# Optimization experiments

Hardware: AMD Instinct MI355X
Metric: run time of the kernel (lower is better)

Reference implementation:

```python
import jax, jax.numpy as jnp
import numpy as np

B, N, F, K, H = 2, 1024, 64, 8, 4
M1 = K + 1                # 9
M2 = (F - 1) * K + 1      # 505
TEMP = 1.0


def setup_inputs() -> dict:
    key = jax.random.key(0)
    ks = jax.random.split(key, 8)
    x = jax.random.normal(ks[0], (B, N, F), dtype=jnp.float32)
    # Bernoulli(0.05) dense adjacency
    adj = (jax.random.uniform(ks[1], (B, N, N)) < 0.05).astype(jnp.float32)
    mask = jnp.ones((B, N), dtype=jnp.float32)
    Wl = jax.random.normal(ks[2], (F, K * H), dtype=jnp.float32) * 0.05
    bl = jnp.zeros((K * H,), dtype=jnp.float32)
    Wr = jax.random.normal(ks[3], (F, K * H), dtype=jnp.float32) * 0.05
    br = jnp.zeros((K * H,), dtype=jnp.float32)
    # fixed affine layer: y = x @ aff_w + aff_b, aff_w[:, :F] = -I, aff_b[M2] = 1
    aff_w = jnp.zeros((F, M1 * M2), dtype=jnp.float32).at[:, :F].set(-jnp.eye(F, dtype=jnp.float32))
    aff_b = jnp.zeros((M1 * M2,), dtype=jnp.float32).at[M2].set(1.0)
    Wm = jax.random.normal(ks[4], (M1 * M2, F), dtype=jnp.float32) * 0.02
    bm = jnp.zeros((F,), dtype=jnp.float32)
    return dict(x=x, adj=adj, mask=mask, Wl=Wl, bl=bl, Wr=Wr, br=br,
                aff_w=aff_w, aff_b=aff_b, Wm=Wm, bm=bm)


def reference(x, adj, mask, Wl, bl, Wr, br, aff_w, aff_b, Wm, bm):
    # --- multi-head edge attention ---
    x_l = (x @ Wl + bl).reshape(B, N, K, H)   # [B,N,K,H]
    x_r = (x @ Wr + br).reshape(B, N, K, H)
    # scores[b,i,j,n,g] = leaky_relu(x_l[b,j] + x_r[b,i]) / temp
    scores = jax.nn.leaky_relu(x_l[:, None, :, :, :] + x_r[:, :, None, :, :]) / TEMP  # [B,N,N,K,H]
    attn_mask = mask[:, None, :] * mask[:, :, None]                # [B,N,N]
    scores = jnp.where(attn_mask[..., None, None] == 0, -1e9, scores)
    att = jax.nn.softmax(scores, axis=2)                           # softmax over source nodes j
    att = jnp.maximum(att * adj[..., None, None], 1e-6)            # clamp(min=1e-6) STE trick
    att = att / jnp.sum(att, axis=2, keepdims=True)                # renormalize
    # --- attention-weighted neighbor gather ---
    x_h = x.reshape(B, N, H, F // H)
    agg = jnp.einsum('bjgk,bijng->bingk', x_h, att).reshape(B, N, K, F)  # [B,N,K,F]
    # --- fixed affine + FFT log-domain geometric mean ---
    x_aff = (agg @ aff_w + aff_b).reshape(B, N, K, M1, M2)
    x_fft = jnp.fft.fft2(x_aff)                                    # over (M1,M2)
    mag = jnp.exp(jnp.mean(jnp.log(jnp.abs(x_fft) + 1e-6), axis=2))  # [B,N,M1,M2]
    ang = jnp.sum(jnp.angle(x_fft), axis=2)
    x_agg = jnp.fft.ifft2(mag * jnp.exp(1j * ang)).real.reshape(B, N, M1 * M2)
    # --- output MLP + node mask ---
    out = x_agg @ Wm + bm
    return out * mask[..., None]
```

## Files before the change

### kernel.cpp

```cpp
#include <hip/hip_runtime.h>
#include <math.h>

#define NN 1024
#define FD 64
#define CH 32
#define M1D 9
#define M2D 505
#define QH 253
#define THALF 2273
#define KPAD 4608
#define KSPLIT 16
#define KCHUNK 288
#define G1SZ 291456
#define G1KS 8

#define FSQRT(x) __builtin_amdgcn_sqrtf(x)
#define FRCP(x)  __builtin_amdgcn_rcpf(x)

typedef short short8 __attribute__((ext_vector_type(8)));
typedef float f32x4 __attribute__((ext_vector_type(4)));

__device__ __forceinline__ unsigned short f2bf(float x) {
    unsigned int u = __builtin_bit_cast(unsigned int, x);
    return (unsigned short)((u + 0x7FFFu + ((u >> 16) & 1u)) >> 16);
}

#define OFF_WP    1024
#define OFF_SUMX  1056
#define OFF_GMT   1184
#define OFF_XL    148640
#define OFF_XR    214176
#define OFF_AGG   279712
#define OFF_PART  1328288
#define OFF_Y     3425440
#define OFF_WT    8144032
#define OFF_G1P   8176800

__global__ __launch_bounds__(256) void build_tw_kernel(float* __restrict__ T,
                                                       float* __restrict__ Wt,
                                                       float* __restrict__ wp,
                                                       float* __restrict__ sumx) {
    int idx = blockIdx.x * 256 + threadIdx.x;
    if (blockIdx.x == 0) {
        if (threadIdx.x < M1D) {
            float ang = (float)threadIdx.x * (-6.2831853f / 9.0f);
            float s, c; __sincosf(ang, &s, &c);
            wp[2*threadIdx.x] = c; wp[2*threadIdx.x+1] = s;
        }
        if (threadIdx.x >= 64 && threadIdx.x < 192) sumx[threadIdx.x - 64] = 0.f;
    }
    if (idx < 506 * 512) {
        int r = idx >> 9, m2 = idx & 511;
        float v = 0.f;
        if (m2 < M2D) {
            int q = r >> 1;
            int t = (q * m2) % M2D;
            float ang = (float)t * (-6.2831853f / 505.0f);
            float s, c; __sincosf(ang, &s, &c);
            v = (r & 1) ? -s : c;
        }
        T[idx] = v;
    } else if (idx < 506 * 512 + 64 * 512) {
        int i2 = idx - 506 * 512;
        int m = i2 >> 9, col = i2 & 511;
        float v = 0.f;
        if (col < 506) {
            int q = col >> 1;
            int t = (q * m) % M2D;
            float ang = (float)t * (-6.2831853f / 505.0f);
            float s, c; __sincosf(ang, &s, &c);
            v = (col & 1) ? s : c;
        }
        Wt[i2] = v;
    }
}

__global__ __launch_bounds__(64) void proj_kernel(const float* __restrict__ x,
                                                  const float* __restrict__ Wl, const float* __restrict__ bl,
                                                  const float* __restrict__ Wr, const float* __restrict__ br,
                                                  float* __restrict__ xl, float* __restrict__ xr,
                                                  float* __restrict__ sumx) {
    int blk = blockIdx.x, tid = threadIdx.x;
    if (blk >= 2048) {
        int bb = blk - 2048;
        int b = bb >> 4, chunk = bb & 15;
        const float* xb = x + (size_t)b * NN * FD;
        float acc = 0.f;
        int j0 = chunk * 64;
        #pragma unroll 4
        for (int j = j0; j < j0 + 64; j++) acc += xb[j*FD + tid];
        atomicAdd(&sumx[b*FD + tid], acc);
        return;
    }
    int node = blk;
    __shared__ float xrow[FD];
    xrow[tid] = x[(size_t)node*FD + tid];
    __syncthreads();
    int c = tid & 31;
    const float* W = (tid < 32) ? Wl : Wr;
    float acc = (tid < 32) ? bl[c] : br[c];
    #pragma unroll
    for (int f = 0; f < FD; f++) acc += xrow[f] * W[f*CH + c];
    float* dst = (tid < 32) ? xl : xr;
    dst[(size_t)node*CH + c] = acc;
}

__global__ __launch_bounds__(256) void g1_gemm_kernel(const float* __restrict__ T,
                                                      const float* __restrict__ Wm,
                                                      float* __restrict__ G1p) {
    int mt = blockIdx.x, m1 = blockIdx.y, ks = blockIdx.z;
    int tid = threadIdx.x;
    __shared__ float As[64][68];
    __shared__ float Bs[64][64];
    int r0 = mt * 64, k0 = ks * 64;
    const float* Wmb = Wm + (size_t)m1 * M2D * FD;
    float ra[16], rb[16];
    #pragma unroll
    for (int i = 0; i < 16; i++) {
        int l = tid + i*256;
        int r = l >> 6, k = l & 63;
        int rr = r0 + r;
        ra[i] = (rr < 506) ? T[(size_t)rr*512 + k0 + k] : 0.f;
    }
    #pragma unroll
    for (int i = 0; i < 16; i++) {
        int l = tid + i*256;
        int k = l >> 6, f = l & 63;
        int krow = k0 + k;
        rb[i] = (krow < M2D) ? Wmb[(size_t)krow*FD + f] : 0.f;
    }
    #pragma unroll
    for (int i = 0; i < 16; i++) {
        int l = tid + i*256;
        As[l & 63][l >> 6] = ra[i];
    }
    #pragma unroll
    for (int i = 0; i < 16; i++) {
        int l = tid + i*256;
        Bs[l >> 6][l & 63] = rb[i];
    }
    __syncthreads();
    float acc[4][4] = {{0.f}};
    int tm = (tid >> 4) * 4, tf = (tid & 15) * 4;
    #pragma unroll 8
    for (int k = 0; k < 64; k++) {
        float4 a = *(const float4*)&As[k][tm];
        float4 b = *(const float4*)&Bs[k][tf];
        acc[0][0] += a.x*b.x; acc[0][1] += a.x*b.y; acc[0][2] += a.x*b.z; acc[0][3] += a.x*b.w;
        acc[1][0] += a.y*b.x; acc[1][1] += a.y*b.y; acc[1][2] += a.y*b.z; acc[1][3] += a.y*b.w;
        acc[2][0] += a.z*b.x; acc[2][1] += a.z*b.y; acc[2][2] += a.z*b.z; acc[2][3] += a.z*b.w;
        acc[3][0] += a.w*b.x; acc[3][1] += a.w*b.y; acc[3][2] += a.w*b.z; acc[3][3] += a.w*b.w;
    }
    float* G1k = G1p + (size_t)ks * G1SZ;
    #pragma unroll
    for (int i = 0; i < 4; i++) {
        int r = r0 + tm + i;
        if (r >= 506) continue;
        int q = r >> 1, reim = r & 1;
        size_t base = (size_t)(m1*QH + q) * 128;
        #pragma unroll
        for (int j = 0; j < 4; j++)
            G1k[base + (tf + j)*2 + reim] = acc[i][j];
    }
}

__global__ __launch_bounds__(64) void gmat_kernel(const float* __restrict__ G1p,
                                                  const float* __restrict__ wp,
                                                  unsigned short* __restrict__ GmT) {
    int t = blockIdx.x;
    int f = threadIdx.x;
    if (t >= THALF) {
        *(unsigned int*)&GmT[(size_t)f*KPAD + 2*t] = 0u;
        return;
    }
    int p, q;
    if (t < QH) { p = 0; q = t; }
    else { int u = t - QH; p = 1 + u / M2D; q = u % M2D; }
    int qq = (q < QH) ? q : (M2D - q);
    float sgn = (q < QH) ? 1.f : -1.f;
    float gr = 0.f, gi = 0.f;
    #pragma unroll
    for (int m1 = 0; m1 < M1D; m1++) {
        size_t o = ((size_t)(m1*QH + qq)*FD + f)*2;
        float ar = 0.f, ai = 0.f;
        #pragma unroll
        for (int ks = 0; ks < G1KS; ks++) {
            ar += G1p[(size_t)ks*G1SZ + o];
            ai += G1p[(size_t)ks*G1SZ + o + 1];
        }
        ai *= sgn;
        int pm = (p * m1) % M1D;
        float cr = wp[2*pm], ci = -wp[2*pm+1];
        gr += ar*cr - ai*ci;
        gi += ar*ci + ai*cr;
    }
    float scale = (t == 0) ? (1.0f/4545.0f) : (2.0f/4545.0f);
    unsigned int pk = (unsigned int)f2bf(gr*scale) | ((unsigned int)f2bf(-gi*scale) << 16);
    *(unsigned int*)&GmT[(size_t)f*KPAD + 2*t] = pk;
}

__global__ __launch_bounds__(256) void attn_agg_kernel(const float* __restrict__ x,
                                                       const float* __restrict__ adj,
                                                       const float* __restrict__ xl,
                                                       const float* __restrict__ xr,
                                                       const float* __restrict__ sumx,
                                                       float* __restrict__ agg) {
    int node = blockIdx.x;
    int b = node >> 10;
    int tid = threadIdx.x;
    __shared__ float xr_s[CH], Zinv[CH], Sinv[CH];
    __shared__ float red16[16][CH];
    __shared__ int act_list[NN + 8];
    __shared__ int act_n;
    __shared__ float qv2[64][CH];

    if (tid < CH) xr_s[tid] = xr[(size_t)node*CH + tid];
    if (tid == 0) act_n = 0;
    __syncthreads();

    int c = tid & 31, jl = tid >> 5;
    const float* xlb = xl + ((size_t)b << 10) * CH;
    const float* adjrow = adj + (size_t)node * NN;

    int c2 = tid & 15, jl16 = tid >> 4;
    const float2* xlb2 = (const float2*)xlb;
    float xrcx = xr_s[2*c2], xrcy = xr_s[2*c2+1];
    float zx = 0.f, zy = 0.f;
    for (int j0 = jl16; j0 < NN; j0 += 128) {
        float2 sv[8];
        #pragma unroll
        for (int u = 0; u < 8; u++) sv[u] = xlb2[(size_t)(j0 + u*16)*16 + c2];
        #pragma unroll
        for (int u = 0; u < 8; u++) {
            float s0 = sv[u].x + xrcx; s0 = s0 > 0.f ? s0 : 0.01f * s0;
            float s1 = sv[u].y + xrcy; s1 = s1 > 0.f ? s1 : 0.01f * s1;
            zx += __expf(s0); zy += __expf(s1);
        }
    }
    red16[jl16][2*c2]   = zx;
    red16[jl16][2*c2+1] = zy;

    float av[4];
    #pragma unroll
    for (int u = 0; u < 4; u++) av[u] = adjrow[tid + u*256];
    __syncthreads();
    if (tid < CH) {
        float z = 0.f;
        #pragma unroll
        for (int r = 0; r < 16; r++) z += red16[r][tid];
        Zinv[tid] = FRCP(z);
    }
    #pragma unroll
    for (int u = 0; u < 4; u++)
        if (av[u] != 0.f) { int p = atomicAdd(&act_n, 1); act_list[p] = tid + u*256; }
    __syncthreads();
    int nact = act_n;

    int f = tid & 63, n0 = tid >> 6;
    int g = f >> 4;
    int c0 = n0*4 + g, c1 = (n0+4)*4 + g;
    const float* xb = x + ((size_t)b << 10) * FD;
    float acc0 = 0.f, acc1 = 0.f, sacc = 0.f;

    for (int base = 0; base < nact; base += 64) {
        int cnt = min(64, nact - base);
        int cntp = (cnt + 7) & ~7;
        for (int u = tid; u < (cnt << 5); u += 256) {
            int jj = u >> 5, cc = u & 31;
            int j = act_list[base + jj];
            float s = xlb[j*CH + cc] + xr_s[cc];
            s = s > 0.f ? s : 0.01f * s;
            float pv = __expf(s) * Zinv[cc];
            float qq = fmaxf(pv, 1e-6f) - 1e-6f;
            qv2[jj][cc] = qq;
            sacc += qq;
        }
        for (int u = tid + (cnt << 5); u < (cntp << 5); u += 256)
            qv2[u >> 5][u & 31] = 0.f;
        if (tid < cntp - cnt) act_list[base + cnt + tid] = act_list[base];
        __syncthreads();
        for (int jb = 0; jb < cntp; jb += 8) {
            float xv[8];
            #pragma unroll
            for (int u = 0; u < 8; u++) xv[u] = xb[act_list[base + jb + u]*FD + f];
            #pragma unroll
            for (int u = 0; u < 8; u++) {
                acc0 += qv2[jb+u][c0] * xv[u];
                acc1 += qv2[jb+u][c1] * xv[u];
            }
        }
        __syncthreads();
    }
    red16[jl][c] = sacc;
    __syncthreads();
    if (tid < CH) {
        float s = 0.f;
        #pragma unroll
        for (int r = 0; r < 8; r++) s += red16[r][tid];
        Sinv[tid] = FRCP(s + (float)NN * 1e-6f);
    }
    __syncthreads();
    float sx = sumx[b*FD + f] * 1e-6f;
    agg[(size_t)node*512 + n0*FD + f]       = (acc0 + sx) * Sinv[c0];
    agg[(size_t)node*512 + (n0+4)*FD + f]   = (acc1 + sx) * Sinv[c1];
}

__global__ __launch_bounds__(256) void ay_kernel(const float* __restrict__ agg,
                                                 const float* __restrict__ Wt,
                                                 unsigned short* __restrict__ Yb) {
    int slab = blockIdx.x, nt = blockIdx.y;
    int tid = threadIdx.x;
    __shared__ float As2[64][68];
    __shared__ float Bs[64][64];
    int tm = (tid >> 4) * 4, tf = (tid & 15) * 4;
    float ra[16], rb[16];
    #pragma unroll
    for (int i = 0; i < 16; i++) {
        int l = tid + i*256;
        int r = l >> 6, k = l & 63;
        ra[i] = agg[(size_t)(slab*64 + r)*64 + k];
    }
    #pragma unroll
    for (int i = 0; i < 16; i++) {
        int l = tid + i*256;
        int k = l >> 6, cc = l & 63;
        rb[i] = Wt[(size_t)k*512 + nt*64 + cc];
    }
    #pragma unroll
    for (int i = 0; i < 16; i++) { int l = tid + i*256; As2[l & 63][l >> 6] = ra[i]; }
    #pragma unroll
    for (int i = 0; i < 16; i++) { int l = tid + i*256; Bs[l >> 6][l & 63] = rb[i]; }
    __syncthreads();
    float acc[4][4] = {{0.f}};
    #pragma unroll 8
    for (int k = 0; k < 64; k++) {
        float4 a = *(const float4*)&As2[k][tm];
        float4 b = *(const float4*)&Bs[k][tf];
        acc[0][0] += a.x*b.x; acc[0][1] += a.x*b.y; acc[0][2] += a.x*b.z; acc[0][3] += a.x*b.w;
        acc[1][0] += a.y*b.x; acc[1][1] += a.y*b.y; acc[1][2] += a.y*b.z; acc[1][3] += a.y*b.w;
        acc[2][0] += a.z*b.x; acc[2][1] += a.z*b.y; acc[2][2] += a.z*b.z; acc[2][3] += a.z*b.w;
        acc[3][0] += a.w*b.x; acc[3][1] += a.w*b.y; acc[3][2] += a.w*b.z; acc[3][3] += a.w*b.w;
    }
    __syncthreads();
    #pragma unroll
    for (int i = 0; i < 4; i++)
        #pragma unroll
        for (int j = 0; j < 4; j++)
            As2[tm + i][tf + j] = acc[i][j];
    __syncthreads();

    int qloc = tid & 31, node = tid >> 5;
    unsigned short* Yrow = Yb + (size_t)(slab*8 + node)*KPAD;
    int q = nt*32 + qloc;

    if (q <= 252) {
        float2 Av[8];
        #pragma unroll
        for (int n = 0; n < 8; n++)
            Av[n] = make_float2(As2[node*8 + n][2*qloc], As2[node*8 + n][2*qloc + 1]);

        const float CPt[5] = {1.0f, 0.766044443119f, 0.173648177667f, -0.5f, -0.939692620786f};
        const float SPt[5] = {0.0f, -0.642787609687f, -0.984807753012f, -0.866025403784f, -0.342020143326f};

        #define Y_PROD(CSIGN, TIDX)                                            \
        {                                                                      \
            float Pr = 1.f, Pi = 0.f, rp2 = 1.f;                               \
            _Pragma("unroll")                                                  \
            for (int n = 0; n < 8; n++) {                                      \
                float Xr = cp - Av[n].x, Xi = sp - (CSIGN) * Av[n].y;          \
                rp2 *= (Xr*Xr + Xi*Xi);                                        \
                float nPr = Pr*Xr - Pi*Xi;                                     \
                Pi = Pr*Xi + Pi*Xr; Pr = nPr;                                  \
            }                                                                  \
            float pAbs = FSQRT(Pr*Pr + Pi*Pi);                                 \
            float rp8 = FSQRT(FSQRT(FSQRT(FSQRT(rp2))));                       \
            float s = rp8 * FRCP(fmaxf(pAbs, 1e-20f));                         \
            unsigned int pk = (unsigned int)f2bf(s*Pr) | ((unsigned int)f2bf(s*Pi) << 16); \
            *(unsigned int*)&Yrow[2*(TIDX)] = pk;                              \
        }

        #pragma unroll
        for (int p = 0; p < 5; p++) {
            float cp = CPt[p], sp = SPt[p];
            int tfwd = (p == 0) ? q : (QH + (p-1)*M2D + q);
            Y_PROD(1.f, tfwd);
            if (p >= 1 && q >= 1) {
                int tmir = QH + (p-1)*M2D + (M2D - q);
                Y_PROD(-1.f, tmir);
            }
        }
        #undef Y_PROD
    }
    if (nt == 7 && tid < 248) {
        int rr = tid / 31, cc2 = tid % 31;
        unsigned short* Yr2 = Yb + (size_t)(slab*8 + rr)*KPAD;
        *(unsigned int*)&Yr2[2*THALF + 2*cc2] = 0u;
    }
}

__global__ __launch_bounds__(256) void gemm_kernel(const unsigned short* __restrict__ Yb,
                                                   const unsigned short* __restrict__ GmT,
                                                   float* __restrict__ part) {
    int mtile = blockIdx.x, kc = blockIdx.y;
    int tid = threadIdx.x;
    __shared__ unsigned short Ys[64*40];
    __shared__ unsigned short Gs[64*40];
    int m0 = mtile * 64;
    int k0 = kc * KCHUNK;
    int r = tid >> 2, kg = (tid & 3) * 8;
    const unsigned short* Ysrc = Yb + (size_t)(m0 + r)*KPAD + k0 + kg;
    const unsigned short* Gsrc = GmT + (size_t)r*KPAD + k0 + kg;
    uint4 ya = *(const uint4*)Ysrc;
    uint4 ga = *(const uint4*)Gsrc;
    int w = tid >> 6, lane = tid & 63;
    int lm = lane & 15, quad = lane >> 4;
    f32x4 acc0 = {0.f,0.f,0.f,0.f}, acc1 = acc0, acc2 = acc0, acc3 = acc0;
    for (int ks = 0; ks < KCHUNK; ks += 32) {
        *(uint4*)&Ys[r*40 + kg] = ya;
        *(uint4*)&Gs[r*40 + kg] = ga;
        __syncthreads();
        if (ks + 32 < KCHUNK) {
            ya = *(const uint4*)(Ysrc + ks + 32);
            ga = *(const uint4*)(Gsrc + ks + 32);
        }
        short8 b  = *(const short8*)&Gs[(w*16 + lm)*40 + quad*8];
        short8 a0 = *(const short8*)&Ys[(lm)*40      + quad*8];
        short8 a1 = *(const short8*)&Ys[(16 + lm)*40 + quad*8];
        short8 a2 = *(const short8*)&Ys[(32 + lm)*40 + quad*8];
        short8 a3 = *(const short8*)&Ys[(48 + lm)*40 + quad*8];
        acc0 = __builtin_amdgcn_mfma_f32_16x16x32_bf16(a0, b, acc0, 0, 0, 0);
        acc1 = __builtin_amdgcn_mfma_f32_16x16x32_bf16(a1, b, acc1, 0, 0, 0);
        acc2 = __builtin_amdgcn_mfma_f32_16x16x32_bf16(a2, b, acc2, 0, 0, 0);
        acc3 = __builtin_amdgcn_mfma_f32_16x16x32_bf16(a3, b, acc3, 0, 0, 0);
        __syncthreads();
    }
    float* prow = part + (size_t)kc * (2048*FD);
    int col = w*16 + lm;
    #pragma unroll
    for (int rr = 0; rr < 4; rr++) {
        int row = quad*4 + rr;
        prow[(size_t)(m0 + row)*FD + col]      = acc0[rr];
        prow[(size_t)(m0 + 16 + row)*FD + col] = acc1[rr];
        prow[(size_t)(m0 + 32 + row)*FD + col] = acc2[rr];
        prow[(size_t)(m0 + 48 + row)*FD + col] = acc3[rr];
    }
}

__global__ __launch_bounds__(256) void reduce_kernel(const float* __restrict__ part,
                                                     const float* __restrict__ bm,
                                                     const float* __restrict__ mask,
                                                     float* __restrict__ out) {
    int idx = blockIdx.x * 256 + threadIdx.x;
    if (idx >= 32768) return;
    const float4* p4 = (const float4*)part;
    float4 s = p4[idx];
    #pragma unroll
    for (int kc = 1; kc < KSPLIT; kc++) {
        float4 v = p4[(size_t)kc*32768 + idx];
        s.x += v.x; s.y += v.y; s.z += v.z; s.w += v.w;
    }
    int f0 = (idx & 15) * 4;
    int node = idx >> 4;
    float mk = mask[node];
    s.x = (s.x + bm[f0])   * mk;
    s.y = (s.y + bm[f0+1]) * mk;
    s.z = (s.z + bm[f0+2]) * mk;
    s.w = (s.w + bm[f0+3]) * mk;
    ((float4*)out)[idx] = s;
}

extern "C" void kernel_launch(void* const* d_in, const int* in_sizes, int n_in,
                              void* d_out, int out_size, void* d_ws, size_t ws_size,
                              hipStream_t stream) {
    const float* x    = (const float*)d_in[0];
    const float* adj  = (const float*)d_in[1];
    const float* mask = (const float*)d_in[2];
    const float* Wl   = (const float*)d_in[3];
    const float* bl   = (const float*)d_in[4];
    const float* Wr   = (const float*)d_in[5];
    const float* br   = (const float*)d_in[6];
    const float* Wm   = (const float*)d_in[9];
    const float* bm   = (const float*)d_in[10];
    float* out = (float*)d_out;
    float* ws  = (float*)d_ws;

    float* wp   = ws + OFF_WP;
    float* sumx = ws + OFF_SUMX;
    unsigned short* GmT = (unsigned short*)(ws + OFF_GMT);
    float* xl   = ws + OFF_XL;
    float* xr   = ws + OFF_XR;
    float* agg  = ws + OFF_AGG;
    float* part = ws + OFF_PART;
    float* T    = ws + OFF_Y;
    unsigned short* Yb = (unsigned short*)(ws + OFF_Y);
    float* Wt   = ws + OFF_WT;
    float* G1p  = ws + OFF_G1P;

    hipLaunchKernelGGL(build_tw_kernel, dim3((506*512 + 64*512 + 255)/256), dim3(256), 0, stream, T, Wt, wp, sumx);
    hipLaunchKernelGGL(proj_kernel, dim3(2080), dim3(64), 0, stream, x, Wl, bl, Wr, br, xl, xr, sumx);
    hipLaunchKernelGGL(g1_gemm_kernel, dim3(8, 9, G1KS), dim3(256), 0, stream, T, Wm, G1p);
    hipLaunchKernelGGL(gmat_kernel, dim3(KPAD/2), dim3(64), 0, stream, G1p, wp, GmT);
    hipLaunchKernelGGL(attn_agg_kernel, dim3(2048), dim3(256), 0, stream, x, adj, xl, xr, sumx, agg);
    hipLaunchKernelGGL(ay_kernel, dim3(256, 8), dim3(256), 0, stream, agg, Wt, Yb);
    hipLaunchKernelGGL(gemm_kernel, dim3(32, KSPLIT), dim3(256), 0, stream, Yb, GmT, part);
    hipLaunchKernelGGL(reduce_kernel, dim3(128), dim3(256), 0, stream, part, bm, mask, out);
}
```

Before: 177.7 us.

## Fuse pipeline into four launches with inline twiddles and atomic split-K output

Eight kernel launches become four. The twiddle-table build moves inline, so twiddles are computed with sincos inside the G1 GEMM and ay tiles. The projection, column-sum, G1 GEMM and output-bias initialisation share one grid, and gmat shares a grid with the attention kernel. The separate split-K reduce kernel is removed: gemm_kernel atomically adds masked partials into an output pre-filled with bias. The intent is to cut launch overhead and intermediate global traffic. The cost is extra transcendental work, float atomic contention, and non-deterministic summation order.

```diff
diff --git a/kernel.cpp b/kernel.cpp
--- a/kernel.cpp
+++ b/kernel.cpp
@@ -25,189 +25,170 @@
     return (unsigned short)((u + 0x7FFFu + ((u >> 16) & 1u)) >> 16);
 }
 
-#define OFF_WP    1024
-#define OFF_SUMX  1056
-#define OFF_GMT   1184
-#define OFF_XL    148640
-#define OFF_XR    214176
-#define OFF_AGG   279712
-#define OFF_PART  1328288
-#define OFF_Y     3425440
-#define OFF_WT    8144032
-#define OFF_G1P   8176800
-
-__global__ __launch_bounds__(256) void build_tw_kernel(float* __restrict__ T,
-                                                       float* __restrict__ Wt,
-                                                       float* __restrict__ wp,
-                                                       float* __restrict__ sumx) {
-    int idx = blockIdx.x * 256 + threadIdx.x;
-    if (blockIdx.x == 0) {
-        if (threadIdx.x < M1D) {
-            float ang = (float)threadIdx.x * (-6.2831853f / 9.0f);
-            float s, c; __sincosf(ang, &s, &c);
-            wp[2*threadIdx.x] = c; wp[2*threadIdx.x+1] = s;
-        }
-        if (threadIdx.x >= 64 && threadIdx.x < 192) sumx[threadIdx.x - 64] = 0.f;
-    }
-    if (idx < 506 * 512) {
-        int r = idx >> 9, m2 = idx & 511;
-        float v = 0.f;
-        if (m2 < M2D) {
-            int q = r >> 1;
-            int t = (q * m2) % M2D;
-            float ang = (float)t * (-6.2831853f / 505.0f);
-            float s, c; __sincosf(ang, &s, &c);
-            v = (r & 1) ? -s : c;
-        }
-        T[idx] = v;
-    } else if (idx < 506 * 512 + 64 * 512) {
-        int i2 = idx - 506 * 512;
-        int m = i2 >> 9, col = i2 & 511;
-        float v = 0.f;
-        if (col < 506) {
-            int q = col >> 1;
-            int t = (q * m) % M2D;
-            float ang = (float)t * (-6.2831853f / 505.0f);
-            float s, c; __sincosf(ang, &s, &c);
-            v = (col & 1) ? s : c;
-        }
-        Wt[i2] = v;
-    }
-}
-
-__global__ __launch_bounds__(64) void proj_kernel(const float* __restrict__ x,
-                                                  const float* __restrict__ Wl, const float* __restrict__ bl,
-                                                  const float* __restrict__ Wr, const float* __restrict__ br,
-                                                  float* __restrict__ xl, float* __restrict__ xr,
-                                                  float* __restrict__ sumx) {
-    int blk = blockIdx.x, tid = threadIdx.x;
-    if (blk >= 2048) {
-        int bb = blk - 2048;
+#define OFF_SUMXP 1024
+#define OFF_GMT   4096
+#define OFF_XL    151552
+#define OFF_XR    217088
+#define OFF_AGG   282624
+#define OFF_Y     1331200
+#define OFF_G1P   6049792
+
+__global__ __launch_bounds__(256) void fused_pre_kernel(
+    const float* __restrict__ x,
+    const float* __restrict__ Wl, const float* __restrict__ bl,
+    const float* __restrict__ Wr, const float* __restrict__ br,
+    const float* __restrict__ Wm, const float* __restrict__ bm,
+    const float* __restrict__ mask,
+    float* __restrict__ xl, float* __restrict__ xr,
+    float* __restrict__ sumxp, float* __restrict__ G1p,
+    float* __restrict__ out)
+{
+    __shared__ float As[64][68];
+    __shared__ float Bs[64][64];
+    int bid = blockIdx.x, tid = threadIdx.x;
+
+    if (bid < 576) {
+        int mt = bid & 7, m1 = (bid >> 3) % 9, ks = bid / 72;
+        int r0 = mt * 64, k0 = ks * 64;
+        const float* Wmb = Wm + (size_t)m1 * M2D * FD;
+        float ra[16], rb[16];
+        #pragma unroll
+        for (int i = 0; i < 16; i++) {
+            int l = tid + i*256;
+            int r = l >> 6, k = l & 63;
+            int rr = r0 + r, m2 = k0 + k;
+            float v = 0.f;
+            if (rr < 506 && m2 < M2D) {
+                int q = rr >> 1;
+                int t = (q * m2) % M2D;
+                float ang = (float)t * (-6.2831853f / 505.0f);
+                float s, c; __sincosf(ang, &s, &c);
+                v = (rr & 1) ? -s : c;
+            }
+            ra[i] = v;
+        }
+        #pragma unroll
+        for (int i = 0; i < 16; i++) {
+            int l = tid + i*256;
+            int k = l >> 6, f = l & 63;
+            int krow = k0 + k;
+            rb[i] = (krow < M2D) ? Wmb[(size_t)krow*FD + f] : 0.f;
+        }
+        #pragma unroll
+        for (int i = 0; i < 16; i++) {
+            int l = tid + i*256;
+            As[l & 63][l >> 6] = ra[i];
+        }
+        #pragma unroll
+        for (int i = 0; i < 16; i++) {
+            int l = tid + i*256;
+            Bs[l >> 6][l & 63] = rb[i];
+        }
+        __syncthreads();
+        float acc[4][4] = {{0.f}};
+        int tm = (tid >> 4) * 4, tf = (tid & 15) * 4;
+        #pragma unroll 8
+        for (int k = 0; k < 64; k++) {
+            float4 a = *(const float4*)&As[k][tm];
+            float4 b = *(const float4*)&Bs[k][tf];
+            acc[0][0] += a.x*b.x; acc[0][1] += a.x*b.y; acc[0][2] += a.x*b.z; acc[0][3] += a.x*b.w;
+            acc[1][0] += a.y*b.x; acc[1][1] += a.y*b.y; acc[1][2] += a.y*b.z; acc[1][3] += a.y*b.w;
+            acc[2][0] += a.z*b.x; acc[2][1] += a.z*b.y; acc[2][2] += a.z*b.z; acc[2][3] += a.z*b.w;
+            acc[3][0] += a.w*b.x; acc[3][1] += a.w*b.y; acc[3][2] += a.w*b.z; acc[3][3] += a.w*b.w;
+        }
+        float* G1k = G1p + (size_t)ks * G1SZ;
+        #pragma unroll
+        for (int i = 0; i < 4; i++) {
+            int r = r0 + tm + i;
+            if (r >= 506) continue;
+            int q = r >> 1, reim = r & 1;
+            size_t base = (size_t)(m1*QH + q) * 128;
+            #pragma unroll
+            for (int j = 0; j < 4; j++)
+                G1k[base + (tf + j)*2 + reim] = acc[i][j];
+        }
+    } else if (bid < 1088) {
+        int grp = tid >> 6, lt = tid & 63;
+        int node = (bid - 576)*4 + grp;
+        float* xrow = &As[0][0] + grp*FD;
+        xrow[lt] = x[(size_t)node*FD + lt];
+        __syncthreads();
+        int c = lt & 31;
+        const float* W = (lt < 32) ? Wl : Wr;
+        float acc = (lt < 32) ? bl[c] : br[c];
+        #pragma unroll
+        for (int f = 0; f < FD; f++) acc += xrow[f] * W[f*CH + c];
+        float* dst = (lt < 32) ? xl : xr;
+        dst[(size_t)node*CH + c] = acc;
+    } else if (bid < 1096) {
+        int bb = (bid - 1088)*4 + (tid >> 6);
+        int f = tid & 63;
         int b = bb >> 4, chunk = bb & 15;
         const float* xb = x + (size_t)b * NN * FD;
         float acc = 0.f;
         int j0 = chunk * 64;
         #pragma unroll 4
-        for (int j = j0; j < j0 + 64; j++) acc += xb[j*FD + tid];
-        atomicAdd(&sumx[b*FD + tid], acc);
+        for (int j = j0; j < j0 + 64; j++) acc += xb[j*FD + f];
+        sumxp[bb*64 + f] = acc;
+    } else {
+        int idx = (bid - 1096)*256 + tid;
+        float4 bv = ((const float4*)bm)[idx & 15];
+        float mk = mask[idx >> 4];
+        bv.x *= mk; bv.y *= mk; bv.z *= mk; bv.w *= mk;
+        ((float4*)out)[idx] = bv;
+    }
+}
+
+__global__ __launch_bounds__(256) void fused_mid_kernel(
+    const float* __restrict__ x, const float* __restrict__ adj,
+    const float* __restrict__ xl, const float* __restrict__ xr,
+    const float* __restrict__ sumxp, const float* __restrict__ G1p,
+    float* __restrict__ agg, unsigned short* __restrict__ GmT)
+{
+    int bid = blockIdx.x, tid = threadIdx.x;
+
+    if (bid >= 2048) {
+        __shared__ float wps[18];
+        if (tid < 9) {
+            float s, c; __sincosf((float)tid * (-6.2831853f / 9.0f), &s, &c);
+            wps[2*tid] = c; wps[2*tid+1] = s;
+        }
+        __syncthreads();
+        int t = (bid - 2048)*4 + (tid >> 6);
+        int f = tid & 63;
+        if (t >= THALF) {
+            *(unsigned int*)&GmT[(size_t)f*KPAD + 2*t] = 0u;
+            return;
+        }
+        int p, q;
+        if (t < QH) { p = 0; q = t; }
+        else { int u = t - QH; p = 1 + u / M2D; q = u % M2D; }
+        int qq = (q < QH) ? q : (M2D - q);
+        float sgn = (q < QH) ? 1.f : -1.f;
+        float gr = 0.f, gi = 0.f;
+        #pragma unroll
+        for (int m1 = 0; m1 < M1D; m1++) {
+            size_t o = ((size_t)(m1*QH + qq)*FD + f)*2;
+            float ar = 0.f, ai = 0.f;
+            #pragma unroll
+            for (int ks = 0; ks < G1KS; ks++) {
+                ar += G1p[(size_t)ks*G1SZ + o];
+                ai += G1p[(size_t)ks*G1SZ + o + 1];
+            }
+            ai *= sgn;
+            int pm = (p * m1) % M1D;
+            float cr = wps[2*pm], ci = -wps[2*pm+1];
+            gr += ar*cr - ai*ci;
+            gi += ar*ci + ai*cr;
+        }
+        float scale = (t == 0) ? (1.0f/4545.0f) : (2.0f/4545.0f);
+        unsigned int pk = (unsigned int)f2bf(gr*scale) | ((unsigned int)f2bf(-gi*scale) << 16);
+        *(unsigned int*)&GmT[(size_t)f*KPAD + 2*t] = pk;
         return;
     }
-    int node = blk;
-    __shared__ float xrow[FD];
-    xrow[tid] = x[(size_t)node*FD + tid];
-    __syncthreads();
-    int c = tid & 31;
-    const float* W = (tid < 32) ? Wl : Wr;
-    float acc = (tid < 32) ? bl[c] : br[c];
-    #pragma unroll
-    for (int f = 0; f < FD; f++) acc += xrow[f] * W[f*CH + c];
-    float* dst = (tid < 32) ? xl : xr;
-    dst[(size_t)node*CH + c] = acc;
-}
-
-__global__ __launch_bounds__(256) void g1_gemm_kernel(const float* __restrict__ T,
-                                                      const float* __restrict__ Wm,
-                                                      float* __restrict__ G1p) {
-    int mt = blockIdx.x, m1 = blockIdx.y, ks = blockIdx.z;
-    int tid = threadIdx.x;
-    __shared__ float As[64][68];
-    __shared__ float Bs[64][64];
-    int r0 = mt * 64, k0 = ks * 64;
-    const float* Wmb = Wm + (size_t)m1 * M2D * FD;
-    float ra[16], rb[16];
-    #pragma unroll
-    for (int i = 0; i < 16; i++) {
-        int l = tid + i*256;
-        int r = l >> 6, k = l & 63;
-        int rr = r0 + r;
-        ra[i] = (rr < 506) ? T[(size_t)rr*512 + k0 + k] : 0.f;
-    }
-    #pragma unroll
-    for (int i = 0; i < 16; i++) {
-        int l = tid + i*256;
-        int k = l >> 6, f = l & 63;
-        int krow = k0 + k;
-        rb[i] = (krow < M2D) ? Wmb[(size_t)krow*FD + f] : 0.f;
-    }
-    #pragma unroll
-    for (int i = 0; i < 16; i++) {
-        int l = tid + i*256;
-        As[l & 63][l >> 6] = ra[i];
-    }
-    #pragma unroll
-    for (int i = 0; i < 16; i++) {
-        int l = tid + i*256;
-        Bs[l >> 6][l & 63] = rb[i];
-    }
-    __syncthreads();
-    float acc[4][4] = {{0.f}};
-    int tm = (tid >> 4) * 4, tf = (tid & 15) * 4;
-    #pragma unroll 8
-    for (int k = 0; k < 64; k++) {
-        float4 a = *(const float4*)&As[k][tm];
-        float4 b = *(const float4*)&Bs[k][tf];
-        acc[0][0] += a.x*b.x; acc[0][1] += a.x*b.y; acc[0][2] += a.x*b.z; acc[0][3] += a.x*b.w;
-        acc[1][0] += a.y*b.x; acc[1][1] += a.y*b.y; acc[1][2] += a.y*b.z; acc[1][3] += a.y*b.w;
-        acc[2][0] += a.z*b.x; acc[2][1] += a.z*b.y; acc[2][2] += a.z*b.z; acc[2][3] += a.z*b.w;
-        acc[3][0] += a.w*b.x; acc[3][1] += a.w*b.y; acc[3][2] += a.w*b.z; acc[3][3] += a.w*b.w;
-    }
-    float* G1k = G1p + (size_t)ks * G1SZ;
-    #pragma unroll
-    for (int i = 0; i < 4; i++) {
-        int r = r0 + tm + i;
-        if (r >= 506) continue;
-        int q = r >> 1, reim = r & 1;
-        size_t base = (size_t)(m1*QH + q) * 128;
-        #pragma unroll
-        for (int j = 0; j < 4; j++)
-            G1k[base + (tf + j)*2 + reim] = acc[i][j];
-    }
-}
-
-__global__ __launch_bounds__(64) void gmat_kernel(const float* __restrict__ G1p,
-                                                  const float* __restrict__ wp,
-                                                  unsigned short* __restrict__ GmT) {
-    int t = blockIdx.x;
-    int f = threadIdx.x;
-    if (t >= THALF) {
-        *(unsigned int*)&GmT[(size_t)f*KPAD + 2*t] = 0u;
-        return;
-    }
-    int p, q;
-    if (t < QH) { p = 0; q = t; }
-    else { int u = t - QH; p = 1 + u / M2D; q = u % M2D; }
-    int qq = (q < QH) ? q : (M2D - q);
-    float sgn = (q < QH) ? 1.f : -1.f;
-    float gr = 0.f, gi = 0.f;
-    #pragma unroll
-    for (int m1 = 0; m1 < M1D; m1++) {
-        size_t o = ((size_t)(m1*QH + qq)*FD + f)*2;
-        float ar = 0.f, ai = 0.f;
-        #pragma unroll
-        for (int ks = 0; ks < G1KS; ks++) {
-            ar += G1p[(size_t)ks*G1SZ + o];
-            ai += G1p[(size_t)ks*G1SZ + o + 1];
-        }
-        ai *= sgn;
-        int pm = (p * m1) % M1D;
-        float cr = wp[2*pm], ci = -wp[2*pm+1];
-        gr += ar*cr - ai*ci;
-        gi += ar*ci + ai*cr;
-    }
-    float scale = (t == 0) ? (1.0f/4545.0f) : (2.0f/4545.0f);
-    unsigned int pk = (unsigned int)f2bf(gr*scale) | ((unsigned int)f2bf(-gi*scale) << 16);
-    *(unsigned int*)&GmT[(size_t)f*KPAD + 2*t] = pk;
-}
-
-__global__ __launch_bounds__(256) void attn_agg_kernel(const float* __restrict__ x,
-                                                       const float* __restrict__ adj,
-                                                       const float* __restrict__ xl,
-                                                       const float* __restrict__ xr,
-                                                       const float* __restrict__ sumx,
-                                                       float* __restrict__ agg) {
-    int node = blockIdx.x;
+
+    int node = bid;
     int b = node >> 10;
-    int tid = threadIdx.x;
     __shared__ float xr_s[CH], Zinv[CH], Sinv[CH];
     __shared__ float red16[16][CH];
     __shared__ int act_list[NN + 8];
@@ -300,13 +281,15 @@
         Sinv[tid] = FRCP(s + (float)NN * 1e-6f);
     }
     __syncthreads();
-    float sx = sumx[b*FD + f] * 1e-6f;
+    float sx = 0.f;
+    #pragma unroll
+    for (int cchunk = 0; cchunk < 16; cchunk++) sx += sumxp[(b*16 + cchunk)*64 + f];
+    sx *= 1e-6f;
     agg[(size_t)node*512 + n0*FD + f]       = (acc0 + sx) * Sinv[c0];
     agg[(size_t)node*512 + (n0+4)*FD + f]   = (acc1 + sx) * Sinv[c1];
 }
 
 __global__ __launch_bounds__(256) void ay_kernel(const float* __restrict__ agg,
-                                                 const float* __restrict__ Wt,
                                                  unsigned short* __restrict__ Yb) {
     int slab = blockIdx.x, nt = blockIdx.y;
     int tid = threadIdx.x;
@@ -324,7 +307,16 @@
     for (int i = 0; i < 16; i++) {
         int l = tid + i*256;
         int k = l >> 6, cc = l & 63;
-        rb[i] = Wt[(size_t)k*512 + nt*64 + cc];
+        int col = nt*64 + cc;
+        float v = 0.f;
+        if (col < 506) {
+            int q = col >> 1;
+            int tt = (q * k) % M2D;
+            float ang = (float)tt * (-6.2831853f / 505.0f);
+            float s, c; __sincosf(ang, &s, &c);
+            v = (col & 1) ? s : c;
+        }
+        rb[i] = v;
     }
     #pragma unroll
     for (int i = 0; i < 16; i++) { int l = tid + i*256; As2[l & 63][l >> 6] = ra[i]; }
@@ -400,7 +392,8 @@
 
 __global__ __launch_bounds__(256) void gemm_kernel(const unsigned short* __restrict__ Yb,
                                                    const unsigned short* __restrict__ GmT,
-                                                   float* __restrict__ part) {
+                                                   const float* __restrict__ mask,
+                                                   float* __restrict__ out) {
     int mtile = blockIdx.x, kc = blockIdx.y;
     int tid = threadIdx.x;
     __shared__ unsigned short Ys[64*40];
@@ -434,39 +427,15 @@
         acc3 = __builtin_amdgcn_mfma_f32_16x16x32_bf16(a3, b, acc3, 0, 0, 0);
         __syncthreads();
     }
-    float* prow = part + (size_t)kc * (2048*FD);
     int col = w*16 + lm;
     #pragma unroll
     for (int rr = 0; rr < 4; rr++) {
-        int row = quad*4 + rr;
-        prow[(size_t)(m0 + row)*FD + col]      = acc0[rr];
-        prow[(size_t)(m0 + 16 + row)*FD + col] = acc1[rr];
-        prow[(size_t)(m0 + 32 + row)*FD + col] = acc2[rr];
-        prow[(size_t)(m0 + 48 + row)*FD + col] = acc3[rr];
-    }
-}
-
-__global__ __launch_bounds__(256) void reduce_kernel(const float* __restrict__ part,
-                                                     const float* __restrict__ bm,
-                                                     const float* __restrict__ mask,
-                                                     float* __restrict__ out) {
-    int idx = blockIdx.x * 256 + threadIdx.x;
-    if (idx >= 32768) return;
-    const float4* p4 = (const float4*)part;
-    float4 s = p4[idx];
-    #pragma unroll
-    for (int kc = 1; kc < KSPLIT; kc++) {
-        float4 v = p4[(size_t)kc*32768 + idx];
-        s.x += v.x; s.y += v.y; s.z += v.z; s.w += v.w;
-    }
-    int f0 = (idx & 15) * 4;
-    int node = idx >> 4;
-    float mk = mask[node];
-    s.x = (s.x + bm[f0])   * mk;
-    s.y = (s.y + bm[f0+1]) * mk;
-    s.z = (s.z + bm[f0+2]) * mk;
-    s.w = (s.w + bm[f0+3]) * mk;
-    ((float4*)out)[idx] = s;
+        int row = m0 + quad*4 + rr;
+        atomicAdd(&out[(size_t)row*FD + col],        acc0[rr] * mask[row]);
+        atomicAdd(&out[(size_t)(row+16)*FD + col],   acc1[rr] * mask[row+16]);
+        atomicAdd(&out[(size_t)(row+32)*FD + col],   acc2[rr] * mask[row+32]);
+        atomicAdd(&out[(size_t)(row+48)*FD + col],   acc3[rr] * mask[row+48]);
+    }
 }
 
 extern "C" void kernel_launch(void* const* d_in, const int* in_sizes, int n_in,
@@ -484,24 +453,18 @@
     float* out = (float*)d_out;
     float* ws  = (float*)d_ws;
 
-    float* wp   = ws + OFF_WP;
-    float* sumx = ws + OFF_SUMX;
+    float* sumxp = ws + OFF_SUMXP;
     unsigned short* GmT = (unsigned short*)(ws + OFF_GMT);
     float* xl   = ws + OFF_XL;
     float* xr   = ws + OFF_XR;
     float* agg  = ws + OFF_AGG;
-    float* part = ws + OFF_PART;
-    float* T    = ws + OFF_Y;
     unsigned short* Yb = (unsigned short*)(ws + OFF_Y);
-    float* Wt   = ws + OFF_WT;
     float* G1p  = ws + OFF_G1P;
 
-    hipLaunchKernelGGL(build_tw_kernel, dim3((506*512 + 64*512 + 255)/256), dim3(256), 0, stream, T, Wt, wp, sumx);
-    hipLaunchKernelGGL(proj_kernel, dim3(2080), dim3(64), 0, stream, x, Wl, bl, Wr, br, xl, xr, sumx);
-    hipLaunchKernelGGL(g1_gemm_kernel, dim3(8, 9, G1KS), dim3(256), 0, stream, T, Wm, G1p);
-    hipLaunchKernelGGL(gmat_kernel, dim3(KPAD/2), dim3(64), 0, stream, G1p, wp, GmT);
-    hipLaunchKernelGGL(attn_agg_kernel, dim3(2048), dim3(256), 0, stream, x, adj, xl, xr, sumx, agg);
-    hipLaunchKernelGGL(ay_kernel, dim3(256, 8), dim3(256), 0, stream, agg, Wt, Yb);
-    hipLaunchKernelGGL(gemm_kernel, dim3(32, KSPLIT), dim3(256), 0, stream, Yb, GmT, part);
-    hipLaunchKernelGGL(reduce_kernel, dim3(128), dim3(256), 0, stream, part, bm, mask, out);
-}
+    hipLaunchKernelGGL(fused_pre_kernel, dim3(1224), dim3(256), 0, stream,
+                       x, Wl, bl, Wr, br, Wm, bm, mask, xl, xr, sumxp, G1p, out);
+    hipLaunchKernelGGL(fused_mid_kernel, dim3(2624), dim3(256), 0, stream,
+                       x, adj, xl, xr, sumxp, G1p, agg, GmT);
+    hipLaunchKernelGGL(ay_kernel, dim3(256, 8), dim3(256), 0, stream, agg, Yb);
+    hipLaunchKernelGGL(gemm_kernel, dim3(32, KSPLIT), dim3(256), 0, stream, Yb, GmT, mask, out);
+}
```

After: 168.5 us. -5.2%, faster.
